# Performance work log

Hardware: AMD Instinct MI355X
Metric: run time of the kernel (lower is better)

Reference implementation:

```python
import jax, jax.numpy as jnp
import numpy as np

B, T, N = 256, 4096, 8   # batch, timesteps, n_actions (state channels = 2n)
H = 64                    # hidden width of the t -> latent_x surrogate MLP
P = 2 * N + 2 * N * N     # params dim: g(n) | mu(n) | Pi(n^2) | Gamma(n^2) = 144
DATA_W, PHYS_W, SUP_W = 1.0, 1.0, 1.0


def setup_inputs() -> dict:
    key = jax.random.key(0)
    ks = jax.random.split(key, 10)
    return {
        "t": jax.random.uniform(ks[0], (B, T), dtype=jnp.float32),
        "x_target": jax.random.normal(ks[1], (B, 2 * N, T), dtype=jnp.float32),
        "params_pred": jax.random.normal(ks[2], (B, P), dtype=jnp.float32) * 0.1,
        "params_target": jax.random.normal(ks[3], (B, P), dtype=jnp.float32) * 0.1,
        "ic_pred": jax.random.normal(ks[4], (B, 2 * N), dtype=jnp.float32),
        "ic_target": jax.random.normal(ks[5], (B, 2 * N), dtype=jnp.float32),
        "W1": jax.random.normal(ks[6], (1, H), dtype=jnp.float32) * 0.5,
        "b1": jax.random.normal(ks[7], (H,), dtype=jnp.float32) * 0.1,
        "W2": jax.random.normal(ks[8], (H, 2 * N), dtype=jnp.float32) * 0.2,
        "b2": jax.random.normal(ks[9], (2 * N,), dtype=jnp.float32) * 0.1,
    }


def _observables(latent, mu, n):
    # compute_observables_torch (assumed): obs = [a, relu(q - mu)], smooth=False
    a = latent[..., :n]
    q = latent[..., n:]
    return jnp.concatenate([a, jax.nn.relu(q - mu)], axis=-1)  # (B,T,2n)


def _rhs(state_T, g, mu, Pi, Gamma, n):
    # preference_dynamics_rhs_torch (assumed):
    #   da/dt = g + Pi @ x - a ;  dx/dt = (Gamma @ a) * (mu - x)
    a = state_T[..., :n]            # (B,T,n)
    x = state_T[..., n:]            # (B,T,n)
    da = g + jnp.einsum('bij,btj->bti', Pi, x) - a
    dx = jnp.einsum('bij,btj->bti', Gamma, a) * (mu - x)
    return jnp.concatenate([da, dx], axis=-1)  # (B,T,2n)


def reference(t, x_target, params_pred, params_target, ic_pred, ic_target, W1, b1, W2, b2):
    n = N
    g = params_pred[:, :n]                                    # (B,n)
    mu = params_pred[:, n:2 * n]                              # (B,n)
    Pi = params_pred[:, 2 * n:2 * n + n * n].reshape(B, n, n)
    Gamma = params_pred[:, 2 * n + n * n:].reshape(B, n, n)
    mu_t = mu[:, None, :]                                     # broadcast over T

    def state_fn(tt):
        # surrogate for the upstream net producing latent_x from t (pointwise in t)
        h = jnp.tanh(tt[..., None] @ W1 + b1)   # (B,T,H)
        latent = h @ W2 + b2                    # (B,T,2n)
        return _observables(latent, mu_t, n)    # (B,T,2n)

    # batched d(state)/dt in ONE forward-mode pass (replaces the T-iteration
    # torch.autograd.grad loop); valid because state[b,τ] depends only on t[b,τ].
    state_T, dstate_dt = jax.jvp(state_fn, (t,), (jnp.ones_like(t),))

    state = jnp.transpose(state_T, (0, 2, 1))                 # (B,2n,T)
    data_loss = jnp.mean((state - x_target) ** 2)

    rhs = _rhs(state_T, g[:, None, :], mu_t, Pi, Gamma, n)
    physics_loss = jnp.mean((dstate_dt - rhs) ** 2)

    pred_pi = jnp.concatenate([params_pred, ic_pred], axis=1)
    tgt_pi = jnp.concatenate([params_target, ic_target], axis=1)
    supervised_loss = jnp.mean((pred_pi - tgt_pi) ** 2)

    return DATA_W * data_loss + PHYS_W * physics_loss + SUP_W * supervised_loss
```

## Files before the change

### kernel.cpp

```cpp
#include <hip/hip_runtime.h>
#include <math.h>

#define B_    256
#define T_    4096
#define N_    8
#define TWON_ 16
#define H_    64
#define P_    144
#define WBLK  64
#define NBLKX (T_ / WBLK)
#define NPART (NBLKX * B_)
#define PSTRIDE 20
#define FBLK  1024

#define INV_MAIN  (1.0f / (float)(B_ * TWON_ * T_))
#define INV_SUP   (1.0f / (float)(B_ * (P_ + TWON_)))

#define TWO_LOG2E 2.8853900817779268f


typedef __fp16   half2_t __attribute__((ext_vector_type(2)));
typedef _Float16 half8_t __attribute__((ext_vector_type(8)));
typedef float    f32x4   __attribute__((ext_vector_type(4)));

union HPack { half2_t h2[4]; half8_t h8; };
union RPack { uint4 u4[4]; half2_t h2[16]; };

__device__ __forceinline__ float wave_reduce(float v) {
    #pragma unroll
    for (int off = 32; off > 0; off >>= 1) v += __shfl_down(v, off, 64);
    return v;
}

__global__ __launch_bounds__(WBLK, 6)
void pinn_main_kernel(const float* __restrict__ t_in,
                      const float* __restrict__ x_target,
                      const float* __restrict__ params_pred,
                      const float* __restrict__ params_target,
                      const float* __restrict__ ic_pred,
                      const float* __restrict__ ic_target,
                      const float* __restrict__ W1,
                      const float* __restrict__ b1,
                      const float* __restrict__ W2,
                      const float* __restrict__ b2,
                      float* __restrict__ partials) {
    __shared__ __align__(16) half2_t spk[WBLK * PSTRIDE];

    const int lane = threadIdx.x;
    const int b    = blockIdx.y;
    const int q    = lane >> 4;
    const int mn   = lane & 15;
    const int k0   = q * 8;

    const float* pp = params_pred + b * P_;
    const int tq = blockIdx.x * WBLK + lane;

    float sup = 0.0f;
    if (blockIdx.x == 0) {
        #pragma unroll
        for (int i = lane; i < P_; i += WBLK) {
            const float d = pp[i] - params_target[b * P_ + i];
            sup = fmaf(d, d, sup);
        }
        if (lane < TWON_) {
            const float d = ic_pred[b * TWON_ + lane] - ic_target[b * TWON_ + lane];
            sup = fmaf(d, d, sup);
        }
    }

    float zwlo[8], zblo[8], zwhi[8], zbhi[8];
    HPack Blo, Bhi, Plo, Phi;
    #pragma unroll
    for (int j2 = 0; j2 < 4; ++j2) {
        const int ka = k0 + 2 * j2, kb = ka + 1;
        const float w1a = W1[ka],      w1b = W1[kb];
        const float w1c = W1[32 + ka], w1d = W1[32 + kb];
        zwlo[2*j2] = TWO_LOG2E * w1a; zwlo[2*j2+1] = TWO_LOG2E * w1b;
        zwhi[2*j2] = TWO_LOG2E * w1c; zwhi[2*j2+1] = TWO_LOG2E * w1d;
        zblo[2*j2] = TWO_LOG2E * b1[ka];      zblo[2*j2+1] = TWO_LOG2E * b1[kb];
        zbhi[2*j2] = TWO_LOG2E * b1[32 + ka]; zbhi[2*j2+1] = TWO_LOG2E * b1[32 + kb];
        const float wa = W2[ka * TWON_ + mn],        wb = W2[kb * TWON_ + mn];
        const float wc = W2[(32 + ka) * TWON_ + mn], wd = W2[(32 + kb) * TWON_ + mn];
        Blo.h2[j2] = __builtin_amdgcn_cvt_pkrtz(wa, wb);
        Bhi.h2[j2] = __builtin_amdgcn_cvt_pkrtz(wc, wd);
        Plo.h2[j2] = __builtin_amdgcn_cvt_pkrtz(w1a * wa, w1b * wb);
        Phi.h2[j2] = __builtin_amdgcn_cvt_pkrtz(w1c * wc, w1d * wd);
    }
    const float b2n = b2[mn];

    const float treg = t_in[b * T_ + tq];

    #pragma unroll
    for (int ti = 0; ti < 4; ++ti) {
        const float tt = __shfl(treg, ti * 16 + mn, 64);

        HPack Ah_lo, Ag_lo, Ah_hi, Ag_hi;
        #pragma unroll
        for (int j2 = 0; j2 < 4; ++j2) {
            float e0 = __builtin_amdgcn_exp2f(fmaf(tt, zwlo[2*j2],   zblo[2*j2]));
            float e1 = __builtin_amdgcn_exp2f(fmaf(tt, zwlo[2*j2+1], zblo[2*j2+1]));
            float r0 = __builtin_amdgcn_rcpf(e0 + 1.0f);
            float r1 = __builtin_amdgcn_rcpf(e1 + 1.0f);
            float h0 = fmaf(-2.0f, r0, 1.0f), h1 = fmaf(-2.0f, r1, 1.0f);
            float g0 = fmaf(-h0, h0, 1.0f),   g1 = fmaf(-h1, h1, 1.0f);
            Ah_lo.h2[j2] = __builtin_amdgcn_cvt_pkrtz(h0, h1);
            Ag_lo.h2[j2] = __builtin_amdgcn_cvt_pkrtz(g0, g1);
            e0 = __builtin_amdgcn_exp2f(fmaf(tt, zwhi[2*j2],   zbhi[2*j2]));
            e1 = __builtin_amdgcn_exp2f(fmaf(tt, zwhi[2*j2+1], zbhi[2*j2+1]));
            r0 = __builtin_amdgcn_rcpf(e0 + 1.0f);
            r1 = __builtin_amdgcn_rcpf(e1 + 1.0f);
            h0 = fmaf(-2.0f, r0, 1.0f); h1 = fmaf(-2.0f, r1, 1.0f);
            g0 = fmaf(-h0, h0, 1.0f);   g1 = fmaf(-h1, h1, 1.0f);
            Ah_hi.h2[j2] = __builtin_amdgcn_cvt_pkrtz(h0, h1);
            Ag_hi.h2[j2] = __builtin_amdgcn_cvt_pkrtz(g0, g1);
        }

        f32x4 lat = {b2n, b2n, b2n, b2n};
        lat = __builtin_amdgcn_mfma_f32_16x16x32_f16(Ah_lo.h8, Blo.h8, lat, 0, 0, 0);
        lat = __builtin_amdgcn_mfma_f32_16x16x32_f16(Ah_hi.h8, Bhi.h8, lat, 0, 0, 0);
        f32x4 dl = {0.0f, 0.0f, 0.0f, 0.0f};
        dl = __builtin_amdgcn_mfma_f32_16x16x32_f16(Ag_lo.h8, Plo.h8, dl, 0, 0, 0);
        dl = __builtin_amdgcn_mfma_f32_16x16x32_f16(Ag_hi.h8, Phi.h8, dl, 0, 0, 0);

        const int rowbase = ti * 16 + 4 * q;
        #pragma unroll
        for (int r = 0; r < 4; ++r) {
            spk[(rowbase + r) * PSTRIDE + mn] = __builtin_amdgcn_cvt_pkrtz(lat[r], dl[r]);
        }
    }

    const float* xt = x_target + (size_t)b * TWON_ * T_ + tq;
    float xtv[TWON_];
    #pragma unroll
    for (int k = 0; k < TWON_; ++k) xtv[k] = xt[(size_t)k * T_];

    __syncthreads();

    float lat[TWON_], dlat[TWON_];
    {
        RPack rp;
        const uint4* pr = (const uint4*)&spk[lane * PSTRIDE];
        #pragma unroll
        for (int c = 0; c < 4; ++c) rp.u4[c] = pr[c];
        #pragma unroll
        for (int i = 0; i < TWON_; ++i) { lat[i] = (float)rp.h2[i].x; dlat[i] = (float)rp.h2[i].y; }
    }

    float a[N_], xs[N_], da_[N_], dxs[N_];
    #pragma unroll
    for (int i = 0; i < N_; ++i) { a[i] = lat[i]; da_[i] = dlat[i]; }
    #pragma unroll
    for (int i = 0; i < N_; ++i) {
        const float qm = lat[N_ + i] - pp[N_ + i];
        xs[i]  = qm > 0.0f ? qm : 0.0f;
        dxs[i] = qm > 0.0f ? dlat[N_ + i] : 0.0f;
    }

    float acc = 0.0f;
    #pragma unroll
    for (int k = 0; k < N_; ++k) { const float d = a[k]  - xtv[k];      acc = fmaf(d, d, acc); }
    #pragma unroll
    for (int k = 0; k < N_; ++k) { const float d = xs[k] - xtv[N_ + k]; acc = fmaf(d, d, acc); }

    const float* Pi  = pp + 2 * N_;
    const float* Gam = pp + 2 * N_ + N_ * N_;
    #pragma unroll
    for (int i = 0; i < N_; ++i) {
        float s1 = pp[i] - a[i];
        #pragma unroll
        for (int j = 0; j < N_; ++j) s1 = fmaf(Pi[i * N_ + j], xs[j], s1);
        float d = da_[i] - s1;
        acc = fmaf(d, d, acc);

        float s2 = 0.0f;
        #pragma unroll
        for (int j = 0; j < N_; ++j) s2 = fmaf(Gam[i * N_ + j], a[j], s2);
        s2 *= (pp[N_ + i] - xs[i]);
        d = dxs[i] - s2;
        acc = fmaf(d, d, acc);
    }

    float v = fmaf(acc, INV_MAIN, sup * INV_SUP);
    float w = wave_reduce(v);
    if (lane == 0) partials[blockIdx.y * gridDim.x + blockIdx.x] = w;
}

__global__ __launch_bounds__(FBLK)
void pinn_finalize_kernel(const float* __restrict__ partials,
                          float* __restrict__ out) {
    __shared__ float swsum[FBLK / 64];
    const int tid = threadIdx.x;

    const float4* p4 = (const float4*)partials;
    float v = 0.0f;
    #pragma unroll
    for (int c = 0; c < 4; ++c) {
        const float4 v4 = p4[tid + c * FBLK];
        v += (v4.x + v4.y) + (v4.z + v4.w);
    }

    float w = wave_reduce(v);
    if ((tid & 63) == 0) swsum[tid >> 6] = w;
    __syncthreads();
    if (tid == 0) {
        float s = 0.0f;
        #pragma unroll
        for (int i = 0; i < FBLK / 64; ++i) s += swsum[i];
        out[0] = s;
    }
}

extern "C" void kernel_launch(void* const* d_in, const int* in_sizes, int n_in,
                              void* d_out, int out_size, void* d_ws, size_t ws_size,
                              hipStream_t stream) {
    const float* t_in          = (const float*)d_in[0];
    const float* x_target      = (const float*)d_in[1];
    const float* params_pred   = (const float*)d_in[2];
    const float* params_target = (const float*)d_in[3];
    const float* ic_pred       = (const float*)d_in[4];
    const float* ic_target     = (const float*)d_in[5];
    const float* W1            = (const float*)d_in[6];
    const float* b1            = (const float*)d_in[7];
    const float* W2            = (const float*)d_in[8];
    const float* b2            = (const float*)d_in[9];
    float* out = (float*)d_out;
    float* partials = (float*)d_ws;

    dim3 grid(NBLKX, B_);
    pinn_main_kernel<<<grid, WBLK, 0, stream>>>(t_in, x_target, params_pred,
                                                params_target, ic_pred, ic_target,
                                                W1, b1, W2, b2, partials);
    pinn_finalize_kernel<<<1, FBLK, 0, stream>>>(partials, out);
}
```

Before: 127.9 us.

## Coalesce x_target loads, fold data loss into MFMA epilogue, pack math

Loads x_target as float4 rows matched to the MFMA output layout, replacing the strided per-thread column loads. The data loss and relu-observable masking now happen in the MFMA epilogue, before the fp16 pack to shared memory. The W1/b1 tanh coefficients are staged in LDS instead of held in 32 registers. The physics matvecs use packed 2-wide float FMAs. The aim is better global load coalescing and lower register pressure, at the cost of an extra barrier and LDS reads. The data-loss term is now computed from fp32 values instead of fp16-rounded ones, so numerics shift slightly.

```diff
diff --git a/kernel.cpp b/kernel.cpp
--- a/kernel.cpp
+++ b/kernel.cpp
@@ -22,6 +22,7 @@
 typedef __fp16   half2_t __attribute__((ext_vector_type(2)));
 typedef _Float16 half8_t __attribute__((ext_vector_type(8)));
 typedef float    f32x4   __attribute__((ext_vector_type(4)));
+typedef float    f32x2   __attribute__((ext_vector_type(2)));
 
 union HPack { half2_t h2[4]; half8_t h8; };
 union RPack { uint4 u4[4]; half2_t h2[16]; };
@@ -45,6 +46,7 @@
                       const float* __restrict__ b2,
                       float* __restrict__ partials) {
     __shared__ __align__(16) half2_t spk[WBLK * PSTRIDE];
+    __shared__ __align__(16) f32x2  szwb[H_];
 
     const int lane = threadIdx.x;
     const int b    = blockIdx.y;
@@ -55,6 +57,20 @@
     const float* pp = params_pred + b * P_;
     const int tq = blockIdx.x * WBLK + lane;
 
+    const float treg = t_in[b * T_ + tq];
+
+    {
+        f32x2 zz = { TWO_LOG2E * W1[lane], TWO_LOG2E * b1[lane] };
+        szwb[lane] = zz;
+    }
+    __syncthreads();
+
+    const float* xrow = x_target + ((size_t)b * TWON_ + mn) * T_
+                        + blockIdx.x * WBLK + q * 4;
+    float4 xt4[4];
+    #pragma unroll
+    for (int i = 0; i < 4; ++i) xt4[i] = *(const float4*)(xrow + i * 16);
+
     float sup = 0.0f;
     if (blockIdx.x == 0) {
         #pragma unroll
@@ -68,17 +84,12 @@
         }
     }
 
-    float zwlo[8], zblo[8], zwhi[8], zbhi[8];
     HPack Blo, Bhi, Plo, Phi;
     #pragma unroll
     for (int j2 = 0; j2 < 4; ++j2) {
         const int ka = k0 + 2 * j2, kb = ka + 1;
         const float w1a = W1[ka],      w1b = W1[kb];
         const float w1c = W1[32 + ka], w1d = W1[32 + kb];
-        zwlo[2*j2] = TWO_LOG2E * w1a; zwlo[2*j2+1] = TWO_LOG2E * w1b;
-        zwhi[2*j2] = TWO_LOG2E * w1c; zwhi[2*j2+1] = TWO_LOG2E * w1d;
-        zblo[2*j2] = TWO_LOG2E * b1[ka];      zblo[2*j2+1] = TWO_LOG2E * b1[kb];
-        zbhi[2*j2] = TWO_LOG2E * b1[32 + ka]; zbhi[2*j2+1] = TWO_LOG2E * b1[32 + kb];
         const float wa = W2[ka * TWON_ + mn],        wb = W2[kb * TWON_ + mn];
         const float wc = W2[(32 + ka) * TWON_ + mn], wd = W2[(32 + kb) * TWON_ + mn];
         Blo.h2[j2] = __builtin_amdgcn_cvt_pkrtz(wa, wb);
@@ -86,101 +97,113 @@
         Plo.h2[j2] = __builtin_amdgcn_cvt_pkrtz(w1a * wa, w1b * wb);
         Phi.h2[j2] = __builtin_amdgcn_cvt_pkrtz(w1c * wc, w1d * wd);
     }
-    const float b2n = b2[mn];
-
-    const float treg = t_in[b * T_ + tq];
+    const float b2n   = b2[mn];
+    const float mucol = pp[mn];
+    const bool  isq   = (mn >= 8);
+
+    float dacc = 0.0f;
 
     #pragma unroll
     for (int ti = 0; ti < 4; ++ti) {
         const float tt = __shfl(treg, ti * 16 + mn, 64);
 
-        HPack Ah_lo, Ag_lo, Ah_hi, Ag_hi;
+        f32x4 lat = {b2n, b2n, b2n, b2n};
+        f32x4 dl  = {0.0f, 0.0f, 0.0f, 0.0f};
+
+        HPack Ah, Ag;
         #pragma unroll
         for (int j2 = 0; j2 < 4; ++j2) {
-            float e0 = __builtin_amdgcn_exp2f(fmaf(tt, zwlo[2*j2],   zblo[2*j2]));
-            float e1 = __builtin_amdgcn_exp2f(fmaf(tt, zwlo[2*j2+1], zblo[2*j2+1]));
-            float r0 = __builtin_amdgcn_rcpf(e0 + 1.0f);
-            float r1 = __builtin_amdgcn_rcpf(e1 + 1.0f);
-            float h0 = fmaf(-2.0f, r0, 1.0f), h1 = fmaf(-2.0f, r1, 1.0f);
-            float g0 = fmaf(-h0, h0, 1.0f),   g1 = fmaf(-h1, h1, 1.0f);
-            Ah_lo.h2[j2] = __builtin_amdgcn_cvt_pkrtz(h0, h1);
-            Ag_lo.h2[j2] = __builtin_amdgcn_cvt_pkrtz(g0, g1);
-            e0 = __builtin_amdgcn_exp2f(fmaf(tt, zwhi[2*j2],   zbhi[2*j2]));
-            e1 = __builtin_amdgcn_exp2f(fmaf(tt, zwhi[2*j2+1], zbhi[2*j2+1]));
-            r0 = __builtin_amdgcn_rcpf(e0 + 1.0f);
-            r1 = __builtin_amdgcn_rcpf(e1 + 1.0f);
-            h0 = fmaf(-2.0f, r0, 1.0f); h1 = fmaf(-2.0f, r1, 1.0f);
-            g0 = fmaf(-h0, h0, 1.0f);   g1 = fmaf(-h1, h1, 1.0f);
-            Ah_hi.h2[j2] = __builtin_amdgcn_cvt_pkrtz(h0, h1);
-            Ag_hi.h2[j2] = __builtin_amdgcn_cvt_pkrtz(g0, g1);
-        }
-
-        f32x4 lat = {b2n, b2n, b2n, b2n};
-        lat = __builtin_amdgcn_mfma_f32_16x16x32_f16(Ah_lo.h8, Blo.h8, lat, 0, 0, 0);
-        lat = __builtin_amdgcn_mfma_f32_16x16x32_f16(Ah_hi.h8, Bhi.h8, lat, 0, 0, 0);
-        f32x4 dl = {0.0f, 0.0f, 0.0f, 0.0f};
-        dl = __builtin_amdgcn_mfma_f32_16x16x32_f16(Ag_lo.h8, Plo.h8, dl, 0, 0, 0);
-        dl = __builtin_amdgcn_mfma_f32_16x16x32_f16(Ag_hi.h8, Phi.h8, dl, 0, 0, 0);
+            const int ka = k0 + 2 * j2;
+            const float4 z = *(const float4*)&szwb[ka];
+            const float e0 = __builtin_amdgcn_exp2f(fmaf(tt, z.x, z.y));
+            const float e1 = __builtin_amdgcn_exp2f(fmaf(tt, z.z, z.w));
+            const float r0 = __builtin_amdgcn_rcpf(e0 + 1.0f);
+            const float r1 = __builtin_amdgcn_rcpf(e1 + 1.0f);
+            const float h0 = fmaf(-2.0f, r0, 1.0f), h1 = fmaf(-2.0f, r1, 1.0f);
+            const float g0 = fmaf(-h0, h0, 1.0f),   g1 = fmaf(-h1, h1, 1.0f);
+            Ah.h2[j2] = __builtin_amdgcn_cvt_pkrtz(h0, h1);
+            Ag.h2[j2] = __builtin_amdgcn_cvt_pkrtz(g0, g1);
+        }
+        lat = __builtin_amdgcn_mfma_f32_16x16x32_f16(Ah.h8, Blo.h8, lat, 0, 0, 0);
+        dl  = __builtin_amdgcn_mfma_f32_16x16x32_f16(Ag.h8, Plo.h8, dl,  0, 0, 0);
+
+        #pragma unroll
+        for (int j2 = 0; j2 < 4; ++j2) {
+            const int ka = k0 + 2 * j2 + 32;
+            const float4 z = *(const float4*)&szwb[ka];
+            const float e0 = __builtin_amdgcn_exp2f(fmaf(tt, z.x, z.y));
+            const float e1 = __builtin_amdgcn_exp2f(fmaf(tt, z.z, z.w));
+            const float r0 = __builtin_amdgcn_rcpf(e0 + 1.0f);
+            const float r1 = __builtin_amdgcn_rcpf(e1 + 1.0f);
+            const float h0 = fmaf(-2.0f, r0, 1.0f), h1 = fmaf(-2.0f, r1, 1.0f);
+            const float g0 = fmaf(-h0, h0, 1.0f),   g1 = fmaf(-h1, h1, 1.0f);
+            Ah.h2[j2] = __builtin_amdgcn_cvt_pkrtz(h0, h1);
+            Ag.h2[j2] = __builtin_amdgcn_cvt_pkrtz(g0, g1);
+        }
+        lat = __builtin_amdgcn_mfma_f32_16x16x32_f16(Ah.h8, Bhi.h8, lat, 0, 0, 0);
+        dl  = __builtin_amdgcn_mfma_f32_16x16x32_f16(Ag.h8, Phi.h8, dl,  0, 0, 0);
 
         const int rowbase = ti * 16 + 4 * q;
+        const float xtr[4] = {xt4[ti].x, xt4[ti].y, xt4[ti].z, xt4[ti].w};
         #pragma unroll
         for (int r = 0; r < 4; ++r) {
-            spk[(rowbase + r) * PSTRIDE + mn] = __builtin_amdgcn_cvt_pkrtz(lat[r], dl[r]);
-        }
-    }
-
-    const float* xt = x_target + (size_t)b * TWON_ * T_ + tq;
-    float xtv[TWON_];
-    #pragma unroll
-    for (int k = 0; k < TWON_; ++k) xtv[k] = xt[(size_t)k * T_];
+            float sv  = lat[r];
+            float dsv = dl[r];
+            const float qm  = sv - mucol;
+            const float svq = fmaxf(qm, 0.0f);
+            const float dsq = qm > 0.0f ? dsv : 0.0f;
+            sv  = isq ? svq : sv;
+            dsv = isq ? dsq : dsv;
+            const float d = sv - xtr[r];
+            dacc = fmaf(d, d, dacc);
+            spk[(rowbase + r) * PSTRIDE + mn] = __builtin_amdgcn_cvt_pkrtz(sv, dsv);
+        }
+    }
 
     __syncthreads();
 
-    float lat[TWON_], dlat[TWON_];
+    RPack rp;
     {
-        RPack rp;
         const uint4* pr = (const uint4*)&spk[lane * PSTRIDE];
         #pragma unroll
         for (int c = 0; c < 4; ++c) rp.u4[c] = pr[c];
-        #pragma unroll
-        for (int i = 0; i < TWON_; ++i) { lat[i] = (float)rp.h2[i].x; dlat[i] = (float)rp.h2[i].y; }
-    }
-
-    float a[N_], xs[N_], da_[N_], dxs[N_];
-    #pragma unroll
-    for (int i = 0; i < N_; ++i) { a[i] = lat[i]; da_[i] = dlat[i]; }
-    #pragma unroll
-    for (int i = 0; i < N_; ++i) {
-        const float qm = lat[N_ + i] - pp[N_ + i];
-        xs[i]  = qm > 0.0f ? qm : 0.0f;
-        dxs[i] = qm > 0.0f ? dlat[N_ + i] : 0.0f;
-    }
-
-    float acc = 0.0f;
-    #pragma unroll
-    for (int k = 0; k < N_; ++k) { const float d = a[k]  - xtv[k];      acc = fmaf(d, d, acc); }
-    #pragma unroll
-    for (int k = 0; k < N_; ++k) { const float d = xs[k] - xtv[N_ + k]; acc = fmaf(d, d, acc); }
+    }
+
+    f32x2 av[4], dav[4], xv[4], dxv[4];
+    #pragma unroll
+    for (int j = 0; j < 4; ++j) {
+        f32x2 t0 = { (float)rp.h2[2*j].x,     (float)rp.h2[2*j+1].x };
+        f32x2 t1 = { (float)rp.h2[2*j].y,     (float)rp.h2[2*j+1].y };
+        f32x2 t2 = { (float)rp.h2[8+2*j].x,   (float)rp.h2[8+2*j+1].x };
+        f32x2 t3 = { (float)rp.h2[8+2*j].y,   (float)rp.h2[8+2*j+1].y };
+        av[j] = t0; dav[j] = t1; xv[j] = t2; dxv[j] = t3;
+    }
 
     const float* Pi  = pp + 2 * N_;
     const float* Gam = pp + 2 * N_ + N_ * N_;
+    float acc = 0.0f;
     #pragma unroll
     for (int i = 0; i < N_; ++i) {
-        float s1 = pp[i] - a[i];
-        #pragma unroll
-        for (int j = 0; j < N_; ++j) s1 = fmaf(Pi[i * N_ + j], xs[j], s1);
-        float d = da_[i] - s1;
-        acc = fmaf(d, d, acc);
-
-        float s2 = 0.0f;
-        #pragma unroll
-        for (int j = 0; j < N_; ++j) s2 = fmaf(Gam[i * N_ + j], a[j], s2);
-        s2 *= (pp[N_ + i] - xs[i]);
-        d = dxs[i] - s2;
-        acc = fmaf(d, d, acc);
-    }
-
-    float v = fmaf(acc, INV_MAIN, sup * INV_SUP);
+        f32x2 s1v = {0.0f, 0.0f};
+        f32x2 s2v = {0.0f, 0.0f};
+        #pragma unroll
+        for (int j = 0; j < 4; ++j) {
+            f32x2 piv = { Pi[i * N_ + 2*j],  Pi[i * N_ + 2*j + 1] };
+            f32x2 gav = { Gam[i * N_ + 2*j], Gam[i * N_ + 2*j + 1] };
+            s1v = __builtin_elementwise_fma(piv, xv[j], s1v);
+            s2v = __builtin_elementwise_fma(gav, av[j], s2v);
+        }
+        const float ai = av[i >> 1][i & 1];
+        const float xi = xv[i >> 1][i & 1];
+        const float s1 = (pp[i] - ai) + (s1v[0] + s1v[1]);
+        const float d1 = dav[i >> 1][i & 1] - s1;
+        acc = fmaf(d1, d1, acc);
+        const float s2 = (s2v[0] + s2v[1]) * (pp[N_ + i] - xi);
+        const float d2 = dxv[i >> 1][i & 1] - s2;
+        acc = fmaf(d2, d2, acc);
+    }
+
+    float v = fmaf(acc + dacc, INV_MAIN, sup * INV_SUP);
     float w = wave_reduce(v);
     if (lane == 0) partials[blockIdx.y * gridDim.x + blockIdx.x] = w;
 }
```

Result: slower. 234.3 us (+83.1%).
